# Kernel optimization log

Measured on AMD Instinct MI355X. Metric: run time of the kernel, lower is better.

Reference implementation:

```python
import jax, jax.numpy as jnp
import numpy as np

STRIDE = 1  # module init arg


def setup_inputs() -> dict:
    key = jax.random.key(0)
    k1, k2 = jax.random.split(key)
    x = jax.random.normal(k1, (16, 32, 256, 256), dtype=jnp.float32)
    kernel = jax.random.normal(k2, (32, 5, 5), dtype=jnp.float32) * 0.1
    return {"input": x, "kernel": kernel}


def _maxmin_conv(x, kernel, stride=STRIDE):
    # Max-min semifield convolution:
    #   out[b,oc,i,j] = max_{c,dy,dx} min(x_pad[b,c,i*s+dy,j*s+dx], k[oc,dy,dx])
    # Since min(., k) is monotone in x, the max over in-channels commutes:
    #   max_{c} min(x_c, k) == min(max_c x_c, k)
    # so we reduce channels once up front (same math, far less memory).
    K = kernel.shape[-1]
    p = K - 1
    top = p // 2
    bot = p - top  # calculate_padding(): left=top=floor(p/2), right=bottom=p-top
    xmax = jnp.max(x, axis=1)  # [B, H, W]
    xp = jnp.pad(xmax, ((0, 0), (top, bot), (top, bot)), constant_values=-np.inf)
    B, Hp, Wp = xp.shape
    Ho = (Hp - K) // stride + 1
    Wo = (Wp - K) // stride + 1
    OC = kernel.shape[0]
    acc = jnp.full((B, OC, Ho, Wo), -np.inf, dtype=x.dtype)
    for dy in range(K):  # fixed small K*K loop over kernel taps
        for dx in range(K):
            patch = xp[:, dy:dy + stride * Ho:stride, dx:dx + stride * Wo:stride]  # [B,Ho,Wo]
            cand = jnp.minimum(patch[:, None, :, :], kernel[None, :, dy, dx, None, None])
            acc = jnp.maximum(acc, cand)
    return acc


def reference(input, kernel):
    return _maxmin_conv(input, kernel)
```

## Files before the change

kernel.cpp:

```cpp
#include <hip/hip_runtime.h>
#include <math.h>


#define BATCH 16
#define CH    32
#define OCH   32
#define HH    256
#define WW    256
#define HWSZ  (HH * WW)
#define TW    32
#define TH    8
#define LH    12
#define LW    42
#define NWG   (BATCH * (HH / TH) * (WW / TW))

typedef float floatx4 __attribute__((ext_vector_type(4)));

__device__ __forceinline__ float vmax3(float a, float b, float c) {
    float d;
    asm("v_max3_f32 %0, %1, %2, %3" : "=v"(d) : "v"(a), "v"(b), "v"(c));
    return d;
}

__global__ __launch_bounds__(256, 2) void fused_maxmin_kernel(const float* __restrict__ x,
                                                              const float* __restrict__ kk,
                                                              float* __restrict__ out) {
    __shared__ float xmt[LH][LW];
    int tid = threadIdx.x;
    int bid = blockIdx.x;
    int swz = (bid & 7) * (NWG >> 3) + (bid >> 3);
    int b   = swz >> 8;
    int t2  = swz & 255;
    int ty  = t2 >> 3;
    int tx  = t2 & 7;

    const float NI = -INFINITY;

    if (tid < 120) {
        int pr = tid / 10;
        int pc = tid % 10;
        int c4 = tx * 8 - 1 + pc;
        int rw = ty * TH - 2 + pr;
        bool valid = (c4 >= 0) && (c4 < WW / 4) && (rw >= 0) && (rw < HH);
        int c4c = c4 < 0 ? 0 : (c4 > WW / 4 - 1 ? WW / 4 - 1 : c4);
        int rwc = rw < 0 ? 0 : (rw > HH - 1 ? HH - 1 : rw);
        const float4* src = (const float4*)x + (size_t)b * CH * (HWSZ / 4)
                          + (size_t)rwc * (WW / 4) + c4c;
        float4 m = src[0];
#pragma unroll
        for (int c = 1; c < CH; ++c) {
            float4 v = src[(size_t)c * (HWSZ / 4)];
            m.x = fmaxf(m.x, v.x);
            m.y = fmaxf(m.y, v.y);
            m.z = fmaxf(m.z, v.z);
            m.w = fmaxf(m.w, v.w);
        }
        if (!valid) { m.x = NI; m.y = NI; m.z = NI; m.w = NI; }
        *(float2*)&xmt[pr][4 * pc]     = make_float2(m.x, m.y);
        *(float2*)&xmt[pr][4 * pc + 2] = make_float2(m.z, m.w);
    }
    __syncthreads();

    int xg = tid & 7;
    int rw = (tid >> 3) & 7;
    int wv = __builtin_amdgcn_readfirstlane(tid >> 6);

    float w[5][8];
#pragma unroll
    for (int r = 0; r < 5; ++r) {
        const float* rp = &xmt[rw + r][4 * xg + 2];
#pragma unroll
        for (int s = 0; s < 4; ++s)
            *(float2*)&w[r][2 * s] = *(const float2*)(rp + 2 * s);
    }

    size_t obase = (size_t)(b * OCH + wv * 8) * HWSZ
                 + (size_t)(ty * TH + rw) * WW + tx * TW + 4 * xg;

    for (int o = 0; o < 8; ++o) {
        const float* kw = kk + (wv * 8 + o) * 25;
        float kr[25];
#pragma unroll
        for (int i = 0; i < 25; ++i) kr[i] = kw[i];

        float a[4];
#pragma unroll
        for (int j = 0; j < 4; ++j) {
            float m[25];
#pragma unroll
            for (int dy = 0; dy < 5; ++dy)
#pragma unroll
                for (int dx = 0; dx < 5; ++dx)
                    m[dy * 5 + dx] = fminf(w[dy][j + dx], kr[dy * 5 + dx]);
            float t0 = vmax3(m[0],  m[1],  m[2]);
            float t1 = vmax3(m[3],  m[4],  m[5]);
            float t2 = vmax3(m[6],  m[7],  m[8]);
            float t3 = vmax3(m[9],  m[10], m[11]);
            float t4 = vmax3(m[12], m[13], m[14]);
            float t5 = vmax3(m[15], m[16], m[17]);
            float t6 = vmax3(m[18], m[19], m[20]);
            float t7 = vmax3(m[21], m[22], m[23]);
            float u0 = vmax3(t0, t1, t2);
            float u1 = vmax3(t3, t4, t5);
            float u2 = vmax3(t6, t7, m[24]);
            a[j] = vmax3(u0, u1, u2);
        }
        floatx4 ov = { a[0], a[1], a[2], a[3] };
        __builtin_nontemporal_store(ov, (floatx4*)(out + obase + (size_t)o * HWSZ));
    }
}

extern "C" void kernel_launch(void* const* d_in, const int* in_sizes, int n_in,
                              void* d_out, int out_size, void* d_ws, size_t ws_size,
                              hipStream_t stream) {
    const float* x  = (const float*)d_in[0];
    const float* kk = (const float*)d_in[1];
    float* out      = (float*)d_out;
    fused_maxmin_kernel<<<NWG, 256, 0, stream>>>(x, kk, out);
}
```

Baseline: 60.25 us.

## Give each wavefront its own tile and all output channels, drop block barrier

Each of the four wavefronts in a workgroup now handles a separate 32x8 spatial tile. It does its own channel-max reduction into a private LDS slice and computes all 32 output channels, so the workgroup-wide __syncthreads is replaced by a wave-local lgkmcnt wait. The grid shrinks to 1024 workgroups, launch bounds rise to 4 waves per SIMD, and kernel weights load as float4 vectors. The aim is to remove barrier stalls and keep more lanes busy during the load phase. In exchange, each wave recomputes its halo independently and runs a longer serial output loop.

```diff
diff --git a/kernel.cpp b/kernel.cpp
--- a/kernel.cpp
+++ b/kernel.cpp
@@ -8,11 +8,9 @@
 #define HH    256
 #define WW    256
 #define HWSZ  (HH * WW)
-#define TW    32
-#define TH    8
 #define LH    12
-#define LW    42
-#define NWG   (BATCH * (HH / TH) * (WW / TW))
+#define LW    44
+#define NWG   1024
 
 typedef float floatx4 __attribute__((ext_vector_type(4)));
 
@@ -22,66 +20,76 @@
     return d;
 }
 
-__global__ __launch_bounds__(256, 2) void fused_maxmin_kernel(const float* __restrict__ x,
+__global__ __launch_bounds__(256, 4) void fused_maxmin_kernel(const float* __restrict__ x,
                                                               const float* __restrict__ kk,
                                                               float* __restrict__ out) {
-    __shared__ float xmt[LH][LW];
-    int tid = threadIdx.x;
-    int bid = blockIdx.x;
-    int swz = (bid & 7) * (NWG >> 3) + (bid >> 3);
-    int b   = swz >> 8;
-    int t2  = swz & 255;
-    int ty  = t2 >> 3;
-    int tx  = t2 & 7;
+    __shared__ float xs[4][LH][LW];
+    int tid  = threadIdx.x;
+    int wv   = tid >> 6;
+    int lane = tid & 63;
+    int bid  = blockIdx.x;
+    int swz  = (bid & 7) * (NWG >> 3) + (bid >> 3);
+    int tile = swz * 4 + wv;
+    int b    = tile >> 8;
+    int t2   = tile & 255;
+    int ty   = t2 >> 3;
+    int tx   = t2 & 7;
+    int row0 = ty * 8;
 
     const float NI = -INFINITY;
+    const float4* xb4 = (const float4*)x + (size_t)b * CH * (HWSZ / 4);
+    float* Ls = &xs[wv][0][0];
 
-    if (tid < 120) {
-        int pr = tid / 10;
-        int pc = tid % 10;
-        int c4 = tx * 8 - 1 + pc;
-        int rw = ty * TH - 2 + pr;
-        bool valid = (c4 >= 0) && (c4 < WW / 4) && (rw >= 0) && (rw < HH);
-        int c4c = c4 < 0 ? 0 : (c4 > WW / 4 - 1 ? WW / 4 - 1 : c4);
-        int rwc = rw < 0 ? 0 : (rw > HH - 1 ? HH - 1 : rw);
-        const float4* src = (const float4*)x + (size_t)b * CH * (HWSZ / 4)
-                          + (size_t)rwc * (WW / 4) + c4c;
-        float4 m = src[0];
 #pragma unroll
-        for (int c = 1; c < CH; ++c) {
-            float4 v = src[(size_t)c * (HWSZ / 4)];
-            m.x = fmaxf(m.x, v.x);
-            m.y = fmaxf(m.y, v.y);
-            m.z = fmaxf(m.z, v.z);
-            m.w = fmaxf(m.w, v.w);
+    for (int gi = 0; gi < 2; ++gi) {
+        int g = lane + 64 * gi;
+        if (g < 120) {
+            int pr = g / 10, pc = g % 10;
+            int c4 = tx * 8 - 1 + pc;
+            int rw = row0 - 2 + pr;
+            bool valid = (c4 >= 0) && (c4 < WW / 4) && (rw >= 0) && (rw < HH);
+            int c4c = c4 < 0 ? 0 : (c4 > WW / 4 - 1 ? WW / 4 - 1 : c4);
+            int rwc = rw < 0 ? 0 : (rw > HH - 1 ? HH - 1 : rw);
+            const float4* src = xb4 + (size_t)rwc * (WW / 4) + c4c;
+            float4 m = src[0];
+#pragma unroll
+            for (int c = 1; c < CH; ++c) {
+                float4 v = src[(size_t)c * (HWSZ / 4)];
+                m.x = fmaxf(m.x, v.x); m.y = fmaxf(m.y, v.y);
+                m.z = fmaxf(m.z, v.z); m.w = fmaxf(m.w, v.w);
+            }
+            if (!valid) { m.x = NI; m.y = NI; m.z = NI; m.w = NI; }
+            *(float4*)(Ls + pr * LW + 4 * pc) = m;
         }
-        if (!valid) { m.x = NI; m.y = NI; m.z = NI; m.w = NI; }
-        *(float2*)&xmt[pr][4 * pc]     = make_float2(m.x, m.y);
-        *(float2*)&xmt[pr][4 * pc + 2] = make_float2(m.z, m.w);
     }
-    __syncthreads();
+    asm volatile("s_waitcnt lgkmcnt(0)" ::: "memory");
 
-    int xg = tid & 7;
-    int rw = (tid >> 3) & 7;
-    int wv = __builtin_amdgcn_readfirstlane(tid >> 6);
-
+    int xg = lane & 7;
+    int rw = lane >> 3;
     float w[5][8];
 #pragma unroll
     for (int r = 0; r < 5; ++r) {
-        const float* rp = &xmt[rw + r][4 * xg + 2];
+        const float* rp = Ls + (rw + r) * LW + 4 * xg + 2;
 #pragma unroll
         for (int s = 0; s < 4; ++s)
             *(float2*)&w[r][2 * s] = *(const float2*)(rp + 2 * s);
     }
 
-    size_t obase = (size_t)(b * OCH + wv * 8) * HWSZ
-                 + (size_t)(ty * TH + rw) * WW + tx * TW + 4 * xg;
+    size_t obase = (size_t)b * OCH * HWSZ + (size_t)(row0 + rw) * WW + tx * 32 + 4 * xg;
 
-    for (int o = 0; o < 8; ++o) {
-        const float* kw = kk + (wv * 8 + o) * 25;
-        float kr[25];
-#pragma unroll
-        for (int i = 0; i < 25; ++i) kr[i] = kw[i];
+#pragma unroll 2
+    for (int o = 0; o < OCH; ++o) {
+        const float* kv = kk + o * 25;
+        float4 q0 = *(const float4*)(kv + 0);
+        float4 q1 = *(const float4*)(kv + 4);
+        float4 q2 = *(const float4*)(kv + 8);
+        float4 q3 = *(const float4*)(kv + 12);
+        float4 q4 = *(const float4*)(kv + 16);
+        float4 q5 = *(const float4*)(kv + 20);
+        float  k24 = kv[24];
+        float kr[25] = { q0.x,q0.y,q0.z,q0.w, q1.x,q1.y,q1.z,q1.w,
+                         q2.x,q2.y,q2.z,q2.w, q3.x,q3.y,q3.z,q3.w,
+                         q4.x,q4.y,q4.z,q4.w, q5.x,q5.y,q5.z,q5.w, k24 };
 
         float a[4];
 #pragma unroll
@@ -100,10 +108,7 @@
             float t5 = vmax3(m[15], m[16], m[17]);
             float t6 = vmax3(m[18], m[19], m[20]);
             float t7 = vmax3(m[21], m[22], m[23]);
-            float u0 = vmax3(t0, t1, t2);
-            float u1 = vmax3(t3, t4, t5);
-            float u2 = vmax3(t6, t7, m[24]);
-            a[j] = vmax3(u0, u1, u2);
+            a[j] = vmax3(vmax3(t0, t1, t2), vmax3(t3, t4, t5), vmax3(t6, t7, m[24]));
         }
         floatx4 ov = { a[0], a[1], a[2], a[3] };
         __builtin_nontemporal_store(ov, (floatx4*)(out + obase + (size_t)o * HWSZ));
```

After: 86.14 us. 1.43x slower.
